# Performance work log

Hardware: AMD Instinct MI355X
Metric: run time of the kernel (lower is better)

## Reference

```python
import jax, jax.numpy as jnp
import numpy as np

H = 16          # num_heads (init kwarg)
EPS = 1e-6      # LayerNorm eps


def rope_freqs(L, d):
    # interleaved RoPE freqs, repeat(f, 'i j -> i (j r)', r=2)
    t = jnp.arange(L, dtype=jnp.float32)
    inv = 1.0 / (10000.0 ** (jnp.arange(0, d, 2, dtype=jnp.float32) / d))
    f = t[:, None] * inv[None, :]          # (L, d//2)
    return jnp.repeat(f, 2, axis=-1)       # (L, d)


def rotate_half(x):
    # pair adjacent elems: (x1, x2) -> (-x2, x1)
    shp = x.shape
    x = x.reshape(shp[:-1] + (shp[-1] // 2, 2))
    x1, x2 = x[..., 0], x[..., 1]
    return jnp.stack((-x2, x1), axis=-1).reshape(shp)


def apply_rope(x, f):
    # x: (B, H, L, d), f: (L, d)
    return x * jnp.cos(f) + rotate_half(x) * jnp.sin(f)


def layernorm(x, g, b):
    m = jnp.mean(x, axis=-1, keepdims=True)
    v = jnp.mean(jnp.square(x - m), axis=-1, keepdims=True)
    return (x - m) * jax.lax.rsqrt(v + EPS) * g + b


def setup_inputs() -> dict:
    key = jax.random.key(0)
    ks = jax.random.split(key, 12)
    B, L, D = 2, 2048, 1024
    Dff = 4 * D
    s = 0.02
    inp = {
        'x': jax.random.normal(ks[0], (B, L, D), jnp.float32),
        'ln1_g': jnp.ones((D,), jnp.float32),
        'ln1_b': jnp.zeros((D,), jnp.float32),
        'wq': jax.random.normal(ks[1], (D, D), jnp.float32) * s,
        'bq': jnp.zeros((D,), jnp.float32),
        'wk': jax.random.normal(ks[2], (D, D), jnp.float32) * s,
        'bk': jnp.zeros((D,), jnp.float32),
        'wv': jax.random.normal(ks[3], (D, D), jnp.float32) * s,
        'bv': jnp.zeros((D,), jnp.float32),
        'wo': jax.random.normal(ks[4], (D, D), jnp.float32) * s,
        'bo': jnp.zeros((D,), jnp.float32),
        'ln2_g': jnp.ones((D,), jnp.float32),
        'ln2_b': jnp.zeros((D,), jnp.float32),
        'w1': jax.random.normal(ks[5], (D, Dff), jnp.float32) * s,
        'b1': jnp.zeros((Dff,), jnp.float32),
        'w2': jax.random.normal(ks[6], (Dff, D), jnp.float32) * s,
        'b2': jnp.zeros((D,), jnp.float32),
        # gates are zero-init in the module; use small random so the block is exercised
        'gate_msa': jax.random.normal(ks[7], (1, 1, D), jnp.float32) * 0.1,
        'gate_mlp': jax.random.normal(ks[8], (1, 1, D), jnp.float32) * 0.1,
    }
    return inp


def reference(x, ln1_g, ln1_b, wq, bq, wk, bk, wv, bv, wo, bo,
              ln2_g, ln2_b, w1, b1, w2, b2, gate_msa, gate_mlp):
    B, L, D = x.shape
    hd = D // H
    # --- self-attention branch ---
    h = layernorm(x, ln1_g, ln1_b)
    q = (h @ wq + bq).reshape(B, L, H, hd).transpose(0, 2, 1, 3)  # (B,H,L,hd)
    k = (h @ wk + bk).reshape(B, L, H, hd).transpose(0, 2, 1, 3)
    v = (h @ wv + bv).reshape(B, L, H, hd).transpose(0, 2, 1, 3)
    f = rope_freqs(L, hd)
    q = apply_rope(q, f)
    k = apply_rope(k, f)
    scores = jnp.einsum('bhic,bhjc->bhij', q, k) / np.float32(np.sqrt(hd))
    attn = jax.nn.softmax(scores, axis=-1)  # dropout disabled (eval)
    o = jnp.einsum('bhij,bhjc->bhic', attn, v)
    o = o.transpose(0, 2, 1, 3).reshape(B, L, D)
    x = x + gate_msa * (o @ wo + bo)
    # --- gated MLP branch ---
    h2 = layernorm(x, ln2_g, ln2_b)
    mlp = jax.nn.gelu(h2 @ w1 + b1, approximate=False) @ w2 + b2
    return x + gate_mlp * mlp
```

## Files before the change

kernel.cpp:

```cpp
#include <hip/hip_runtime.h>

typedef unsigned short u16;
typedef __attribute__((ext_vector_type(4))) float f32x4;
typedef __attribute__((ext_vector_type(8))) short bf16x8;

#define DEV static __device__ __forceinline__

DEV float bf2f(u16 u) { unsigned int i = ((unsigned int)u) << 16; return __builtin_bit_cast(float, i); }
DEV u16 f2bf(float f) {
  unsigned int x = __builtin_bit_cast(unsigned int, f);
  x += 0x7fffu + ((x >> 16) & 1u);
  return (u16)(x >> 16);
}

DEV unsigned cvtpk(float lo, float hi) {
  unsigned r;
  asm("v_cvt_pk_bf16_f32 %0, %1, %2" : "=v"(r) : "v"(lo), "v"(hi));
  return r;
}
DEV float exp2a(float x) {
  float r;
  asm("v_exp_f32 %0, %1" : "=v"(r) : "v"(x));
  return r;
}

DEV void gload16(const u16* g, u16* l) {
  __builtin_amdgcn_global_load_lds(
      (const __attribute__((address_space(1))) unsigned int*)g,
      (__attribute__((address_space(3))) unsigned int*)l, 16, 0, 0);
}

__global__ __launch_bounds__(256) void ln_k(const float* __restrict__ x,
                                            const float* __restrict__ g,
                                            const float* __restrict__ b,
                                            u16* __restrict__ out) {
  const int row = blockIdx.x;
  const int t = threadIdx.x;
  const float4 v = *(const float4*)(x + (size_t)row * 1024 + t * 4);
  float s = v.x + v.y + v.z + v.w;
  float q = v.x * v.x + v.y * v.y + v.z * v.z + v.w * v.w;
#pragma unroll
  for (int m = 1; m < 64; m <<= 1) { s += __shfl_xor(s, m); q += __shfl_xor(q, m); }
  __shared__ float ss[4], qs[4];
  if ((t & 63) == 0) { ss[t >> 6] = s; qs[t >> 6] = q; }
  __syncthreads();
  s = ss[0] + ss[1] + ss[2] + ss[3];
  q = qs[0] + qs[1] + qs[2] + qs[3];
  const float mean = s * (1.0f / 1024.0f);
  const float var = q * (1.0f / 1024.0f) - mean * mean;
  const float rs = rsqrtf(var + 1e-6f);
  const float4 gv = *(const float4*)(g + t * 4);
  const float4 bv = *(const float4*)(b + t * 4);
  ushort4 o;
  o.x = f2bf((v.x - mean) * rs * gv.x + bv.x);
  o.y = f2bf((v.y - mean) * rs * gv.y + bv.y);
  o.z = f2bf((v.z - mean) * rs * gv.z + bv.z);
  o.w = f2bf((v.w - mean) * rs * gv.w + bv.w);
  *(ushort4*)(out + (size_t)row * 1024 + t * 4) = o;
}

__global__ __launch_bounds__(256) void tcvt_k(const float* __restrict__ src,
                                              u16* __restrict__ dst, int K, int N) {
  __shared__ u16 tl[32][33];
  const int k0 = blockIdx.x * 32, n0 = blockIdx.y * 32;
  const int c = threadIdx.x & 31, r0 = threadIdx.x >> 5;
#pragma unroll
  for (int p = 0; p < 4; p++) {
    const int r = p * 8 + r0;
    tl[r][c] = f2bf(src[(size_t)(k0 + r) * N + n0 + c]);
  }
  __syncthreads();
#pragma unroll
  for (int p = 0; p < 4; p++) {
    const int r = p * 8 + r0;
    dst[(size_t)(n0 + r) * K + k0 + c] = tl[c][r];
  }
}

template <int EPI, int TN>
__global__ __launch_bounds__(256) void gemm_bt(const u16* __restrict__ A,
                                               const u16* __restrict__ Bt,
                                               const float* __restrict__ bias,
                                               const float* __restrict__ resid,
                                               const float* __restrict__ gate,
                                               void* __restrict__ outv,
                                               int M, int N, int K) {
  constexpr int MI = (TN == 128) ? 4 : 2;
  constexpr int WRS = (TN == 128) ? 64 : 32;
  __shared__ __align__(16) u16 lA[2][128 * 32];
  __shared__ __align__(16) u16 lB[2][TN * 32];
  const int tid = threadIdx.x;
  const int lane = tid & 63, wid = tid >> 6;
  const int l4 = lane >> 4, l15 = lane & 15;
  const int wr = (TN == 128) ? (wid >> 1) : wid;
  const int wc = (TN == 128) ? (wid & 1) : 0;
  const int mBase = blockIdx.x * 128;
  const int nBase = blockIdx.y * TN;

  f32x4 acc[MI][4];
#pragma unroll
  for (int i = 0; i < MI; i++)
#pragma unroll
    for (int j = 0; j < 4; j++)
#pragma unroll
      for (int e = 0; e < 4; e++) acc[i][j][e] = 0.f;

  const int sRow = tid >> 2;
  const int sCol = (tid & 3) * 8;

#define STAGE(bufi, k0)                                                               \
  {                                                                                   \
    _Pragma("unroll") for (int p = 0; p < 2; p++)                                     \
        gload16(A + (size_t)(mBase + p * 64 + sRow) * K + (k0) + sCol,                \
                &lA[bufi][p * 2048 + wid * 512]);                                     \
    _Pragma("unroll") for (int p = 0; p < TN / 64; p++)                               \
        gload16(Bt + (size_t)(nBase + p * 64 + sRow) * K + (k0) + sCol,               \
                &lB[bufi][p * 2048 + wid * 512]);                                     \
  }

  const int nt = K >> 5;
  STAGE(0, 0);
  __syncthreads();
  int buf = 0;
  for (int it = 0; it < nt; ++it) {
    if (it + 1 < nt) STAGE(buf ^ 1, (it + 1) * 32);
    bf16x8 af[MI], bfr[4];
#pragma unroll
    for (int mi = 0; mi < MI; mi++)
      af[mi] = *(const bf16x8*)(&lA[buf][(wr * WRS + mi * 16 + l15) * 32 + l4 * 8]);
#pragma unroll
    for (int ni = 0; ni < 4; ni++)
      bfr[ni] = *(const bf16x8*)(&lB[buf][(wc * 64 + ni * 16 + l15) * 32 + l4 * 8]);
#pragma unroll
    for (int mi = 0; mi < MI; mi++)
#pragma unroll
      for (int ni = 0; ni < 4; ni++)
        acc[mi][ni] = __builtin_amdgcn_mfma_f32_16x16x32_bf16(af[mi], bfr[ni], acc[mi][ni], 0, 0, 0);
    __syncthreads();
    buf ^= 1;
  }
#undef STAGE

  u16* obf = (u16*)outv;
  float* of = (float*)outv;
#pragma unroll
  for (int mi = 0; mi < MI; mi++) {
#pragma unroll
    for (int ni = 0; ni < 4; ni++) {
      const int row0 = mBase + wr * WRS + mi * 16 + l4 * 4;
      const int col = nBase + wc * 64 + ni * 16 + l15;
      const float bb = bias[col];
#pragma unroll
      for (int r = 0; r < 4; r++) {
        const float v = acc[mi][ni][r] + bb;
        const size_t idx = (size_t)(row0 + r) * N + col;
        if (EPI == 0) {
          obf[idx] = f2bf(v);
        } else if (EPI == 1) {
          const float ge = 0.5f * v * (1.0f + erff(v * 0.70710678118654752f));
          obf[idx] = f2bf(ge);
        } else if (EPI == 2) {
          of[idx] = resid[idx] + gate[col] * v;
        } else {
          of[idx] = of[idx] + gate[col] * v;
        }
      }
    }
  }
}

__global__ __launch_bounds__(256) void rope_k(const u16* __restrict__ qkv,
                                              u16* __restrict__ qr, u16* __restrict__ kr) {
  const int sel = blockIdx.y;
  const int rid = blockIdx.x * 8 + (threadIdx.x >> 5);
  const int i = threadIdx.x & 31;
  const int b = rid >> 15;
  const int h = (rid >> 11) & 15;
  const int t = rid & 2047;
  const u16* src = qkv + (size_t)(b * 2048 + t) * 3072 + sel * 1024 + h * 64 + 2 * i;
  const ushort2 uv = *(const ushort2*)src;
  const float x0 = bf2f(uv.x), x1 = bf2f(uv.y);
  const float inv = __expf(-(float)i * 0.28782313662425572f);
  float sn, cs;
  sincosf((float)t * inv, &sn, &cs);
  const float sc = sel ? 1.0f : 0.18033688011112042f;
  ushort2 ov;
  ov.x = f2bf((x0 * cs - x1 * sn) * sc);
  ov.y = f2bf((x1 * cs + x0 * sn) * sc);
  *(ushort2*)((sel ? kr : qr) + (size_t)rid * 64 + 2 * i) = ov;
}

__global__ __launch_bounds__(256) void vtrans_k(const u16* __restrict__ qkv, u16* __restrict__ vt) {
  __shared__ u16 tl[64][65];
  const int bh = blockIdx.x >> 5;
  const int t0 = (blockIdx.x & 31) * 64;
  const int b = bh >> 4, h = bh & 15;
  const int tid = threadIdx.x;
#pragma unroll
  for (int p = 0; p < 16; p++) {
    const int e = p * 256 + tid;
    const int tr = e >> 6, d = e & 63;
    tl[tr][d] = qkv[(size_t)(b * 2048 + t0 + tr) * 3072 + 2048 + h * 64 + d];
  }
  __syncthreads();
#pragma unroll
  for (int p = 0; p < 16; p++) {
    const int e = p * 256 + tid;
    const int dr = e >> 6, tc = e & 63;
    vt[(size_t)(bh * 64 + dr) * 2048 + t0 + tc] = tl[tc][dr];
  }
}

__global__ __launch_bounds__(256) void attn_k(const u16* __restrict__ q,
                                              const u16* __restrict__ k,
                                              const u16* __restrict__ vt,
                                              u16* __restrict__ o) {
  const int bh = blockIdx.y;
  const int tid = threadIdx.x;
  const int wid = tid >> 6, lane = tid & 63;
  const int l4 = lane >> 4, l15 = lane & 15;
  const int qrow0 = blockIdx.x * 128 + wid * 32;

  __shared__ __align__(16) u16 kls[2][4096];
  __shared__ __align__(16) u16 vls[2][4096];
  __shared__ __align__(16) u16 pls[4][2048];
  __shared__ __align__(16) float alds[4][32];

  const size_t qoff = ((size_t)bh * 2048 + qrow0) * 64;
  bf16x8 qf[2][2];
#pragma unroll
  for (int g = 0; g < 2; g++) {
    qf[g][0] = *(const bf16x8*)(q + qoff + (size_t)(g * 16 + l15) * 64 + l4 * 8);
    qf[g][1] = *(const bf16x8*)(q + qoff + (size_t)(g * 16 + l15) * 64 + 32 + l4 * 8);
  }

  float m0 = -1e30f, m1 = -1e30f, ls0 = 0.f, ls1 = 0.f;
  f32x4 oacc[2][4];
#pragma unroll
  for (int g = 0; g < 2; g++)
#pragma unroll
    for (int ni = 0; ni < 4; ni++)
#pragma unroll
      for (int e = 0; e < 4; e++) oacc[g][ni][e] = 0.f;

  const char* kg = (const char*)(k + (size_t)bh * 2048 * 64);
  const char* vg = (const char*)(vt + (size_t)bh * 64 * 2048);
  const int sA = tid, sB = 256 + tid;
  const int rA = sA >> 3, cA = ((sA & 7) ^ (rA & 7)) << 4;
  const int rB = sB >> 3, cB = ((sB & 7) ^ (rB & 7)) << 4;
  u16* kd0 = &kls[0][(size_t)(wid * 64) * 8];
  u16* kd1 = &kls[0][(size_t)(256 + wid * 64) * 8];
  u16* vd0 = &vls[0][(size_t)(wid * 64) * 8];
  u16* vd1 = &vls[0][(size_t)(256 + wid * 64) * 8];

#define STAGE(bufi, kv0)                                                            \
  {                                                                                 \
    const int _o = (bufi)*4096;                                                     \
    gload16((const u16*)(kg + (size_t)((kv0) + rA) * 128 + cA), kd0 + _o);          \
    gload16((const u16*)(kg + (size_t)((kv0) + rB) * 128 + cB), kd1 + _o);          \
    gload16((const u16*)(vg + (size_t)rA * 4096 + (kv0)*2 + cA), vd0 + _o);         \
    gload16((const u16*)(vg + (size_t)rB * 4096 + (kv0)*2 + cB), vd1 + _o);         \
  }

  STAGE(0, 0);
  __syncthreads();

  char* P = (char*)pls[wid];
  float* AL = alds[wid];
  char* prow0 = P + l15 * 128;
  char* prow1 = P + (16 + l15) * 128;
  const int psw = (l15 & 7) << 4;

  int buf = 0;
  for (int it = 0; it < 32; ++it) {
    if (it < 31) STAGE(buf ^ 1, (it + 1) * 64);
    const char* K = (const char*)kls[buf];
    const char* V = (const char*)vls[buf];

    f32x4 s0[4], s1[4];
#pragma unroll
    for (int kt = 0; kt < 4; kt++) {
      const int row = kt * 16 + l15;
      const int sw = (row & 7) << 4;
      const char* kr = K + row * 128;
      const bf16x8 kf0 = *(const bf16x8*)(kr + ((l4 * 16) ^ sw));
      const bf16x8 kf1 = *(const bf16x8*)(kr + ((64 + l4 * 16) ^ sw));
      f32x4 z0 = {0.f, 0.f, 0.f, 0.f}, z1 = {0.f, 0.f, 0.f, 0.f};
      z0 = __builtin_amdgcn_mfma_f32_16x16x32_bf16(kf0, qf[0][0], z0, 0, 0, 0);
      s0[kt] = __builtin_amdgcn_mfma_f32_16x16x32_bf16(kf1, qf[0][1], z0, 0, 0, 0);
      z1 = __builtin_amdgcn_mfma_f32_16x16x32_bf16(kf0, qf[1][0], z1, 0, 0, 0);
      s1[kt] = __builtin_amdgcn_mfma_f32_16x16x32_bf16(kf1, qf[1][1], z1, 0, 0, 0);
    }

    float a00 = fmaxf(fmaxf(s0[0][0], s0[0][1]), fmaxf(s0[0][2], s0[0][3]));
    float a01 = fmaxf(fmaxf(s0[1][0], s0[1][1]), fmaxf(s0[1][2], s0[1][3]));
    float a02 = fmaxf(fmaxf(s0[2][0], s0[2][1]), fmaxf(s0[2][2], s0[2][3]));
    float a03 = fmaxf(fmaxf(s0[3][0], s0[3][1]), fmaxf(s0[3][2], s0[3][3]));
    float pm0 = fmaxf(fmaxf(a00, a01), fmaxf(a02, a03));
    float a10 = fmaxf(fmaxf(s1[0][0], s1[0][1]), fmaxf(s1[0][2], s1[0][3]));
    float a11 = fmaxf(fmaxf(s1[1][0], s1[1][1]), fmaxf(s1[1][2], s1[1][3]));
    float a12 = fmaxf(fmaxf(s1[2][0], s1[2][1]), fmaxf(s1[2][2], s1[2][3]));
    float a13 = fmaxf(fmaxf(s1[3][0], s1[3][1]), fmaxf(s1[3][2], s1[3][3]));
    float pm1 = fmaxf(fmaxf(a10, a11), fmaxf(a12, a13));
    pm0 = fmaxf(pm0, __shfl_xor(pm0, 16));
    pm0 = fmaxf(pm0, __shfl_xor(pm0, 32));
    pm1 = fmaxf(pm1, __shfl_xor(pm1, 16));
    pm1 = fmaxf(pm1, __shfl_xor(pm1, 32));
    const bool need = !__all((pm0 <= m0 + 11.54f) && (pm1 <= m1 + 11.54f));
    float al0 = 1.0f, al1 = 1.0f;
    if (need) {
      const float mn0 = fmaxf(m0, pm0), mn1 = fmaxf(m1, pm1);
      al0 = exp2a(m0 - mn0); al1 = exp2a(m1 - mn1);
      m0 = mn0; m1 = mn1;
      if (l4 == 0) { AL[l15] = al0; AL[16 + l15] = al1; }
    }
#pragma unroll
    for (int kt = 0; kt < 4; kt++)
#pragma unroll
      for (int r = 0; r < 4; r++) {
        s0[kt][r] = exp2a(s0[kt][r] - m0);
        s1[kt][r] = exp2a(s1[kt][r] - m1);
      }
    float e00 = (s0[0][0] + s0[0][1]) + (s0[0][2] + s0[0][3]);
    float e01 = (s0[1][0] + s0[1][1]) + (s0[1][2] + s0[1][3]);
    float e02 = (s0[2][0] + s0[2][1]) + (s0[2][2] + s0[2][3]);
    float e03 = (s0[3][0] + s0[3][1]) + (s0[3][2] + s0[3][3]);
    float ps0 = (e00 + e01) + (e02 + e03);
    float e10 = (s1[0][0] + s1[0][1]) + (s1[0][2] + s1[0][3]);
    float e11 = (s1[1][0] + s1[1][1]) + (s1[1][2] + s1[1][3]);
    float e12 = (s1[2][0] + s1[2][1]) + (s1[2][2] + s1[2][3]);
    float e13 = (s1[3][0] + s1[3][1]) + (s1[3][2] + s1[3][3]);
    float ps1 = (e10 + e11) + (e12 + e13);
    ps0 += __shfl_xor(ps0, 16); ps0 += __shfl_xor(ps0, 32);
    ps1 += __shfl_xor(ps1, 16); ps1 += __shfl_xor(ps1, 32);
    ls0 = ls0 * al0 + ps0;
    ls1 = ls1 * al1 + ps1;

#pragma unroll
    for (int kt = 0; kt < 4; kt++) {
      uint2 w0, w1;
      w0.x = cvtpk(s0[kt][0], s0[kt][1]);
      w0.y = cvtpk(s0[kt][2], s0[kt][3]);
      w1.x = cvtpk(s1[kt][0], s1[kt][1]);
      w1.y = cvtpk(s1[kt][2], s1[kt][3]);
      *(uint2*)(prow0 + ((kt * 32 + l4 * 8) ^ psw)) = w0;
      *(uint2*)(prow1 + ((kt * 32 + l4 * 8) ^ psw)) = w1;
    }
    asm volatile("s_waitcnt lgkmcnt(0)" ::: "memory");
    const bf16x8 pa00 = *(const bf16x8*)(prow0 + ((l4 * 16) ^ psw));
    const bf16x8 pa01 = *(const bf16x8*)(prow0 + ((64 + l4 * 16) ^ psw));
    const bf16x8 pa10 = *(const bf16x8*)(prow1 + ((l4 * 16) ^ psw));
    const bf16x8 pa11 = *(const bf16x8*)(prow1 + ((64 + l4 * 16) ^ psw));
    if (need) {
      const f32x4 a0 = *(const f32x4*)((const char*)AL + l4 * 16);
      const f32x4 a1 = *(const f32x4*)((const char*)AL + 64 + l4 * 16);
#pragma unroll
      for (int ni = 0; ni < 4; ni++) { oacc[0][ni] *= a0; oacc[1][ni] *= a1; }
    }

#pragma unroll
    for (int ni = 0; ni < 4; ni++) {
      const int vrow = ni * 16 + l15;
      const int vsw = (vrow & 7) << 4;
      const char* vr = V + vrow * 128;
      const bf16x8 v0 = *(const bf16x8*)(vr + ((l4 * 16) ^ vsw));
      const bf16x8 v1 = *(const bf16x8*)(vr + ((64 + l4 * 16) ^ vsw));
      oacc[0][ni] = __builtin_amdgcn_mfma_f32_16x16x32_bf16(pa00, v0, oacc[0][ni], 0, 0, 0);
      oacc[0][ni] = __builtin_amdgcn_mfma_f32_16x16x32_bf16(pa01, v1, oacc[0][ni], 0, 0, 0);
      oacc[1][ni] = __builtin_amdgcn_mfma_f32_16x16x32_bf16(pa10, v0, oacc[1][ni], 0, 0, 0);
      oacc[1][ni] = __builtin_amdgcn_mfma_f32_16x16x32_bf16(pa11, v1, oacc[1][ni], 0, 0, 0);
    }
    __syncthreads();
    buf ^= 1;
  }
#undef STAGE

  if (l4 == 0) { AL[l15] = 1.0f / ls0; AL[16 + l15] = 1.0f / ls1; }
  asm volatile("s_waitcnt lgkmcnt(0)" ::: "memory");
  const f32x4 iv0 = *(const f32x4*)((const char*)AL + l4 * 16);
  const f32x4 iv1 = *(const f32x4*)((const char*)AL + 64 + l4 * 16);
  const int b = bh >> 4, h = bh & 15;
#pragma unroll
  for (int g = 0; g < 2; g++) {
#pragma unroll
    for (int r = 0; r < 4; r++) {
      const size_t row = (size_t)b * 2048 + qrow0 + g * 16 + l4 * 4 + r;
      const float iv = g ? iv1[r] : iv0[r];
#pragma unroll
      for (int ni = 0; ni < 4; ni++)
        o[row * 1024 + h * 64 + ni * 16 + l15] = f2bf(oacc[g][ni][r] * iv);
    }
  }
}

extern "C" void kernel_launch(void* const* d_in, const int* in_sizes, int n_in,
                              void* d_out, int out_size, void* d_ws, size_t ws_size,
                              hipStream_t stream) {
  (void)in_sizes; (void)n_in; (void)out_size; (void)ws_size;
  const float* x     = (const float*)d_in[0];
  const float* ln1_g = (const float*)d_in[1];
  const float* ln1_b = (const float*)d_in[2];
  const float* wq    = (const float*)d_in[3];
  const float* bq    = (const float*)d_in[4];
  const float* wk    = (const float*)d_in[5];
  const float* bk    = (const float*)d_in[6];
  const float* wv    = (const float*)d_in[7];
  const float* bv    = (const float*)d_in[8];
  const float* wo    = (const float*)d_in[9];
  const float* bo    = (const float*)d_in[10];
  const float* ln2_g = (const float*)d_in[11];
  const float* ln2_b = (const float*)d_in[12];
  const float* w1    = (const float*)d_in[13];
  const float* b1    = (const float*)d_in[14];
  const float* w2    = (const float*)d_in[15];
  const float* b2    = (const float*)d_in[16];
  const float* gmsa  = (const float*)d_in[17];
  const float* gmlp  = (const float*)d_in[18];
  float* out = (float*)d_out;

  char* w = (char*)d_ws;
  auto alloc = [&](size_t bytes) {
    char* p = w;
    w += (bytes + 255) & ~(size_t)255;
    return p;
  };
  u16* h1     = (u16*)alloc(4096UL * 1024 * 2);
  u16* wqkv_t = (u16*)alloc(3072UL * 1024 * 2);
  u16* wo_t   = (u16*)alloc(1024UL * 1024 * 2);
  u16* w1_t   = (u16*)alloc(4096UL * 1024 * 2);
  u16* w2_t   = (u16*)alloc(1024UL * 4096 * 2);
  float* bqkv = (float*)alloc(3072UL * 4);
  u16* qkv    = (u16*)alloc(4096UL * 3072 * 2);
  u16* q_r    = (u16*)alloc(65536UL * 64 * 2);
  u16* k_r    = (u16*)alloc(65536UL * 64 * 2);
  u16* v_t    = (u16*)alloc(65536UL * 64 * 2);
  u16* o_at   = (u16*)alloc(4096UL * 1024 * 2);
  u16* h2     = (u16*)alloc(4096UL * 1024 * 2);
  u16* g1     = (u16*)alloc(4096UL * 4096 * 2);

  tcvt_k<<<dim3(32, 32), 256, 0, stream>>>(wq, wqkv_t, 1024, 1024);
  tcvt_k<<<dim3(32, 32), 256, 0, stream>>>(wk, wqkv_t + 1024 * 1024, 1024, 1024);
  tcvt_k<<<dim3(32, 32), 256, 0, stream>>>(wv, wqkv_t + 2048 * 1024, 1024, 1024);
  tcvt_k<<<dim3(32, 32), 256, 0, stream>>>(wo, wo_t, 1024, 1024);
  tcvt_k<<<dim3(32, 128), 256, 0, stream>>>(w1, w1_t, 1024, 4096);
  tcvt_k<<<dim3(128, 32), 256, 0, stream>>>(w2, w2_t, 4096, 1024);
  hipMemcpyAsync(bqkv,        bq, 1024 * sizeof(float), hipMemcpyDeviceToDevice, stream);
  hipMemcpyAsync(bqkv + 1024, bk, 1024 * sizeof(float), hipMemcpyDeviceToDevice, stream);
  hipMemcpyAsync(bqkv + 2048, bv, 1024 * sizeof(float), hipMemcpyDeviceToDevice, stream);

  ln_k<<<4096, 256, 0, stream>>>(x, ln1_g, ln1_b, h1);
  gemm_bt<0, 128><<<dim3(32, 24), 256, 0, stream>>>(h1, wqkv_t, bqkv, nullptr, nullptr, qkv, 4096, 3072, 1024);
  rope_k<<<dim3(8192, 2), 256, 0, stream>>>(qkv, q_r, k_r);
  vtrans_k<<<1024, 256, 0, stream>>>(qkv, v_t);
  attn_k<<<dim3(16, 32), 256, 0, stream>>>(q_r, k_r, v_t, o_at);
  gemm_bt<2, 64><<<dim3(32, 16), 256, 0, stream>>>(o_at, wo_t, bo, x, gmsa, out, 4096, 1024, 1024);

  ln_k<<<4096, 256, 0, stream>>>(out, ln2_g, ln2_b, h2);
  gemm_bt<1, 128><<<dim3(32, 32), 256, 0, stream>>>(h2, w1_t, b1, nullptr, nullptr, g1, 4096, 4096, 1024);
  gemm_bt<3, 64><<<dim3(32, 16), 256, 0, stream>>>(g1, w2_t, b2, nullptr, gmlp, out, 4096, 1024, 4096);
}
```

Measured before the change: 312.6 us.

## Triple-buffer GEMM LDS tiles with vmcnt-based waits instead of syncthreads

The bf16 GEMM main loop moves from double to triple buffering in LDS, prefetching two K-tiles ahead with direct global-to-LDS loads. Full __syncthreads drains are replaced by explicit s_waitcnt vmcnt(N) that waits only for the older tile, followed by a raw s_barrier. The goal is to keep global loads in flight across iterations and hide memory latency behind MFMA work. This raises LDS usage per block, which may reduce occupancy, and the hand-counted vmcnt values must exactly match the number of loads issued per stage.

```diff
diff --git a/kernel.cpp b/kernel.cpp
--- a/kernel.cpp
+++ b/kernel.cpp
@@ -22,6 +22,14 @@
   float r;
   asm("v_exp_f32 %0, %1" : "=v"(r) : "v"(x));
   return r;
+}
+
+template <int N>
+DEV void wait_vmcnt() {
+  if constexpr (N == 0) asm volatile("s_waitcnt vmcnt(0)" ::: "memory");
+  else if constexpr (N == 3) asm volatile("s_waitcnt vmcnt(3)" ::: "memory");
+  else if constexpr (N == 4) asm volatile("s_waitcnt vmcnt(4)" ::: "memory");
+  else static_assert(N == 0, "unsupported vmcnt");
 }
 
 DEV void gload16(const u16* g, u16* l) {
@@ -87,8 +95,9 @@
                                                int M, int N, int K) {
   constexpr int MI = (TN == 128) ? 4 : 2;
   constexpr int WRS = (TN == 128) ? 64 : 32;
-  __shared__ __align__(16) u16 lA[2][128 * 32];
-  __shared__ __align__(16) u16 lB[2][TN * 32];
+  constexpr int L = 2 + TN / 64;
+  __shared__ __align__(16) u16 lA[3][128 * 32];
+  __shared__ __align__(16) u16 lB[3][TN * 32];
   const int tid = threadIdx.x;
   const int lane = tid & 63, wid = tid >> 6;
   const int l4 = lane >> 4, l15 = lane & 15;
@@ -120,24 +129,38 @@
 
   const int nt = K >> 5;
   STAGE(0, 0);
-  __syncthreads();
-  int buf = 0;
+  STAGE(1, 32);
+  wait_vmcnt<L>();
+  __builtin_amdgcn_s_barrier();
+  __builtin_amdgcn_sched_barrier(0);
+
+  int bsel = 0;
   for (int it = 0; it < nt; ++it) {
-    if (it + 1 < nt) STAGE(buf ^ 1, (it + 1) * 32);
     bf16x8 af[MI], bfr[4];
 #pragma unroll
     for (int mi = 0; mi < MI; mi++)
-      af[mi] = *(const bf16x8*)(&lA[buf][(wr * WRS + mi * 16 + l15) * 32 + l4 * 8]);
+      af[mi] = *(const bf16x8*)(&lA[bsel][(wr * WRS + mi * 16 + l15) * 32 + l4 * 8]);
 #pragma unroll
     for (int ni = 0; ni < 4; ni++)
-      bfr[ni] = *(const bf16x8*)(&lB[buf][(wc * 64 + ni * 16 + l15) * 32 + l4 * 8]);
+      bfr[ni] = *(const bf16x8*)(&lB[bsel][(wc * 64 + ni * 16 + l15) * 32 + l4 * 8]);
+    if (it + 2 < nt) {
+      int b2 = bsel + 2; if (b2 >= 3) b2 -= 3;
+      STAGE(b2, (it + 2) * 32);
+    }
 #pragma unroll
     for (int mi = 0; mi < MI; mi++)
 #pragma unroll
       for (int ni = 0; ni < 4; ni++)
         acc[mi][ni] = __builtin_amdgcn_mfma_f32_16x16x32_bf16(af[mi], bfr[ni], acc[mi][ni], 0, 0, 0);
-    __syncthreads();
-    buf ^= 1;
+    if (it + 1 < nt) {
+      asm volatile("s_waitcnt lgkmcnt(0)" ::: "memory");
+      __builtin_amdgcn_sched_barrier(0);
+      if (it + 2 < nt) wait_vmcnt<L>();
+      else wait_vmcnt<0>();
+      __builtin_amdgcn_s_barrier();
+      __builtin_amdgcn_sched_barrier(0);
+    }
+    bsel = (bsel == 2) ? 0 : bsel + 1;
   }
 #undef STAGE
 
```

Result: faster. 289.8 us (-7.3%).
